# Performance work log

Hardware: AMD Instinct MI355X
Metric: run time of the kernel (lower is better)

Reference implementation:

```python
import jax, jax.numpy as jnp
import numpy as np

N_SITES = 1024
N_SYMM = 1024
ALPHA_SYMM = 16  # alpha * n_sites / n_symm with alpha=16


def logcosh(x):
    # numerically stable log(cosh(x)) = |x| + log1p(exp(-2|x|)) - log(2)
    ax = jnp.abs(x)
    return ax + jnp.log1p(jnp.exp(-2.0 * ax)) - jnp.log(2.0)


def setup_inputs() -> dict:
    key = jax.random.key(0)
    k1, k2, k3, k4 = jax.random.split(key, 4)
    x_in = jax.random.normal(k1, (4096, N_SITES), dtype=jnp.float32)
    Wsymm = jax.random.normal(k2, (N_SITES, ALPHA_SYMM), dtype=jnp.float32) * 0.1
    bsymm = jax.random.normal(k3, (ALPHA_SYMM,), dtype=jnp.float32) * 0.1
    v_bias = jax.random.normal(k4, (1,), dtype=jnp.float32) * 0.1
    # cyclic translation group: perm_i[k] = (k + i) mod n_sites
    perms = (np.arange(N_SITES)[:, None] + np.arange(N_SITES)[None, :]) % N_SITES
    perms = jnp.asarray(perms, dtype=jnp.int32)  # [n_symm, n_sites]
    return {"x_in": x_in, "Wsymm": Wsymm, "bsymm": bsymm, "v_bias": v_bias, "perms": perms}


def reference(x_in, Wsymm, bsymm, v_bias, perms):
    n_symm, n_sites = perms.shape
    # expand_kernel: kernel[i, j*n_sites + k] = Wsymm[perms[i, k], j]
    # Wsymm[perms] -> [n_symm, n_sites, alpha_symm]; transpose and flatten -> [n_symm, alpha_symm*n_sites]
    kernel = jnp.transpose(Wsymm[perms], (0, 2, 1)).reshape(n_symm, -1)
    # expand_bias: repeat each bsymm[j] n_symm times -> [alpha_symm*n_symm]
    bias = jnp.repeat(bsymm, n_symm)
    y = x_in @ kernel + bias  # [batch, n_hidden]
    y = jnp.sum(logcosh(y), axis=-1)  # [batch]
    y = y + v_bias[0] * jnp.sum(x_in, axis=-1)
    return y
```

## Files before the change

kernel.cpp:

```cpp
#include <hip/hip_runtime.h>
#include <hip/hip_bf16.h>
#include <math.h>

#define LN2F 0.6931471805599453f
#define SCL 9.765625e-4f
#define TWO_OVER_LN2 2.885390081777927f

typedef __attribute__((ext_vector_type(2))) float f32x2;


#define LSW(s) ((s) ^ (((s) >> 4) & 15))

__device__ __forceinline__ f32x2 mk2(float x, float y) { f32x2 r; r.x = x; r.y = y; return r; }

__device__ __forceinline__ f32x2 cmul(f32x2 a, f32x2 b) {
  return a.xx * b + mk2(-a.y, a.y) * b.yx;
}

__device__ __forceinline__ f32x2 pk_cmul(f32x2 a, f32x2 b) {
  f32x2 d, t;
  asm("v_pk_mul_f32 %1, %2, %3 op_sel:[0,0] op_sel_hi:[0,1]\n\t"
      "v_pk_fma_f32 %0, %2, %3, %1 op_sel:[1,1,0] op_sel_hi:[1,0,1] neg_lo:[1,0,0]"
      : "=v"(d), "=&v"(t) : "v"(a), "v"(b));
  return d;
}
__device__ __forceinline__ f32x2 pk_cmulj(f32x2 a, f32x2 b) {
  f32x2 d, t;
  asm("v_pk_mul_f32 %1, %2, %3 op_sel:[0,0] op_sel_hi:[0,1] neg_hi:[0,1]\n\t"
      "v_pk_fma_f32 %0, %2, %3, %1 op_sel:[1,1,0] op_sel_hi:[1,0,1]"
      : "=v"(d), "=&v"(t) : "v"(a), "v"(b));
  return d;
}
__device__ __forceinline__ f32x2 pk_add(f32x2 a, f32x2 b) {
  f32x2 o;
  asm("v_pk_add_f32 %0, %1, %2" : "=v"(o) : "v"(a), "v"(b));
  return o;
}
__device__ __forceinline__ f32x2 pk_sub(f32x2 a, f32x2 b) {
  f32x2 o;
  asm("v_pk_add_f32 %0, %1, %2 neg_lo:[0,1] neg_hi:[0,1]" : "=v"(o) : "v"(a), "v"(b));
  return o;
}
__device__ __forceinline__ f32x2 pk_addrot_p(f32x2 a, f32x2 d) {
  f32x2 o;
  asm("v_pk_add_f32 %0, %1, %2 op_sel:[0,1] op_sel_hi:[1,0] neg_lo:[0,1]"
      : "=v"(o) : "v"(a), "v"(d));
  return o;
}
__device__ __forceinline__ f32x2 pk_addrot_m(f32x2 a, f32x2 d) {
  f32x2 o;
  asm("v_pk_add_f32 %0, %1, %2 op_sel:[0,1] op_sel_hi:[1,0] neg_hi:[0,1]"
      : "=v"(o) : "v"(a), "v"(d));
  return o;
}
__device__ __forceinline__ f32x2 pk_nabs(f32x2 a) {
  return mk2(fabsf(a.x), fabsf(a.y));
}

__device__ __forceinline__ float fast_exp2(float x) {
#if __has_builtin(__builtin_amdgcn_exp2f)
  return __builtin_amdgcn_exp2f(x);
#else
  return exp2f(x);
#endif
}
__device__ __forceinline__ float fast_log2(float x) {
#if __has_builtin(__builtin_amdgcn_logf)
  return __builtin_amdgcn_logf(x);
#else
  return __log2f(x);
#endif
}

__device__ __forceinline__ f32x2 Ctw(int m) {
  switch (m) {
    case 0:   return mk2(1.f, 0.f);
    case 1:   return mk2(0.999981175f, -0.006135885f);
    case 2:   return mk2(0.999924702f, -0.012271538f);
    case 3:   return mk2(0.999830582f, -0.018406730f);
    case 64:  return mk2(0.923879533f, -0.382683432f);
    case 128: return mk2(0.707106781f, -0.707106781f);
    case 192: return mk2(0.382683432f, -0.923879533f);
    case 256: return mk2(0.f, -1.f);
    case 384: return mk2(-0.707106781f, -0.707106781f);
    case 576: return mk2(-0.923879533f, 0.382683432f);
  }
  return mk2(1.f, 0.f);
}

#define BFLY_F(x0,x1,x2,x3,W1,W2,W3,y0,y1,y2,y3) do { \
  f32x2 t0 = x0+x2, t1 = x1+x3, t2 = x0-x2, d_ = x1-x3; \
  f32x2 t3 = mk2(d_.y, -d_.x); \
  y0 = t0+t1; y1 = cmul(t2+t3, W1); \
  y2 = cmul(t0-t1, W2); y3 = cmul(t2-t3, W3); } while(0)

#define BFLY_I(x0,x1,x2,x3,W1,W2,W3,y0,y1,y2,y3) do { \
  f32x2 u1 = pk_cmulj(x1,W1), u2 = pk_cmulj(x2,W2), u3 = pk_cmulj(x3,W3); \
  f32x2 t0 = pk_add(x0,u2), t1 = pk_add(u1,u3), t2 = pk_sub(x0,u2), d_ = pk_sub(u1,u3); \
  y0 = pk_add(t0,t1); y1 = pk_addrot_p(t2,d_); \
  y2 = pk_sub(t0,t1); y3 = pk_addrot_m(t2,d_); } while(0)

#define BFLY_I1(x0,x1,x2,x3,y0,y1,y2,y3) do { \
  f32x2 t0 = pk_add(x0,x2), t1 = pk_add(x1,x3), t2 = pk_sub(x0,x2), d_ = pk_sub(x1,x3); \
  y0 = pk_add(t0,t1); y1 = pk_addrot_p(t2,d_); \
  y2 = pk_sub(t0,t1); y3 = pk_addrot_m(t2,d_); } while(0)

__global__ void k_twiddle(f32x2* __restrict__ tw) {
  int m = blockIdx.x * 256 + threadIdx.x;
  float th = (float)(2.0 * M_PI / 1024.0) * (float)m;
  tw[m] = mk2(cosf(th), -sinf(th));
}

__global__ __launch_bounds__(256, 3) void k_fft_fwd(
    const float* __restrict__ src, int estride, int rstride,
    const f32x2* __restrict__ tw, f32x2* __restrict__ dst, float scale,
    const float* __restrict__ vbias, float* __restrict__ out, int dorow) {
  __shared__ __align__(16) f32x2 fft[4][1024];
  int tid = threadIdx.x, wv = tid >> 6, u = tid & 63;
  int row = blockIdx.x * 4 + wv;
  const float* xr = src + (size_t)row * rstride;
  f32x2* L = fft[wv];
  f32x2 twu = tw[u];
  f32x2 tw4u = tw[4 * u];
  int tp = u & 3;
  f32x2 tw16t = tw[16 * tp], tw64t = tw[64 * tp];

  float vr[4][4]; float rs = 0.f;
  #pragma unroll
  for (int a = 0; a < 4; ++a)
    #pragma unroll
    for (int k = 0; k < 4; ++k) {
      float s = xr[(u + 64 * a + 256 * k) * estride];
      vr[a][k] = s; rs += s;
    }
  f32x2 v[4][4];
  #pragma unroll
  for (int a = 0; a < 4; ++a) {
    float x0 = vr[a][0], x1 = vr[a][1], x2 = vr[a][2], x3 = vr[a][3];
    float t0 = x0 + x2, t1 = x1 + x3, t2 = x0 - x2, dm = x1 - x3;
    f32x2 W1 = cmul(twu, Ctw(64 * a));
    f32x2 W2 = cmul(W1, W1), W3 = cmul(W1, W2);
    v[a][0] = mk2(t0 + t1, 0.f);
    v[a][1] = cmul(mk2(t2, -dm), W1);
    v[a][2] = cmul(mk2(t0 - t1, 0.f), W2);
    v[a][3] = cmul(mk2(t2, dm), W3);
  }
  {
    f32x2 W1 = tw4u, W2 = cmul(W1, W1), W3 = cmul(W1, W2);
    #pragma unroll
    for (int k = 0; k < 4; ++k) {
      f32x2 y0,y1,y2,y3;
      BFLY_F(v[0][k], v[1][k], v[2][k], v[3][k], W1, W2, W3, y0,y1,y2,y3);
      v[0][k]=y0; v[1][k]=y1; v[2][k]=y2; v[3][k]=y3;
    }
  }
  #pragma unroll
  for (int a = 0; a < 4; ++a)
    #pragma unroll
    for (int k = 0; k < 4; ++k)
      L[LSW(u + 64 * a + 256 * k)] = v[a][k];

  int D = u >> 2;
  f32x2 w[4][4];
  #pragma unroll
  for (int c = 0; c < 4; ++c)
    #pragma unroll
    for (int ap = 0; ap < 4; ++ap)
      w[c][ap] = L[LSW(64 * D + 16 * c + 4 * ap + tp)];
  #pragma unroll
  for (int ap = 0; ap < 4; ++ap) {
    f32x2 W1 = cmul(Ctw(64 * ap), tw16t);
    f32x2 W2 = cmul(W1, W1), W3 = cmul(W1, W2);
    f32x2 y0,y1,y2,y3;
    BFLY_F(w[0][ap], w[1][ap], w[2][ap], w[3][ap], W1, W2, W3, y0,y1,y2,y3);
    w[0][ap]=y0; w[1][ap]=y1; w[2][ap]=y2; w[3][ap]=y3;
  }
  {
    f32x2 W1 = tw64t, W2 = cmul(W1, W1), W3 = cmul(W1, W2);
    #pragma unroll
    for (int c = 0; c < 4; ++c) {
      f32x2 y0,y1,y2,y3;
      BFLY_F(w[c][0], w[c][1], w[c][2], w[c][3], W1, W2, W3, y0,y1,y2,y3);
      w[c][0]=y0; w[c][1]=y1; w[c][2]=y2; w[c][3]=y3;
    }
  }
  #pragma unroll
  for (int c = 0; c < 4; ++c)
    #pragma unroll
    for (int ap = 0; ap < 4; ++ap)
      L[LSW(64 * D + 16 * c + 4 * ap + tp)] = w[c][ap];

  f32x2* drow = dst + (size_t)row * 1024;
  #pragma unroll
  for (int j = 0; j < 4; ++j) {
    f32x2 z0 = L[LSW(16 * u + 4 * j)];
    f32x2 z1 = L[LSW(16 * u + 4 * j + 1)];
    f32x2 z2 = L[LSW(16 * u + 4 * j + 2)];
    f32x2 z3 = L[LSW(16 * u + 4 * j + 3)];
    f32x2 t0 = z0+z2, t1 = z1+z3, t2 = z0-z2, d = z1-z3;
    f32x2 t3 = mk2(d.y, -d.x);
    f32x2 y0 = (t0+t1)*scale, y1 = (t2+t3)*scale, y2 = (t0-t1)*scale, y3 = (t2-t3)*scale;
    float4* dp = (float4*)(drow + 16 * u + 4 * j);
    dp[0] = make_float4(y0.x, y0.y, y1.x, y1.y);
    dp[1] = make_float4(y2.x, y2.y, y3.x, y3.y);
  }
  if (dorow) {
    #pragma unroll
    for (int m = 32; m; m >>= 1) rs += __shfl_down(rs, m);
    if (u == 0) out[row] = vbias[0] * rs;
  }
}


#define PW(M, XA, XB, ZA, ZB) do { \
  float4 qa = W0p[M], qb = W1p[M]; \
  f32x2 g1 = pk_cmulj(mk2(qa.x,qa.y), XA); \
  f32x2 g2 = pk_cmulj(mk2(qb.x,qb.y), XA); \
  ZA = pk_addrot_p(g1, g2); \
  g1 = pk_cmulj(mk2(qa.z,qa.w), XB); \
  g2 = pk_cmulj(mk2(qb.z,qb.w), XB); \
  ZB = pk_addrot_p(g1, g2); } while(0)

#define QP_A(P, LPA) do { \
  const float4* W0p = (const float4*)(Wfs + (size_t)(2*(P)) * 1024 + s16); \
  const float4* W1p = (const float4*)(Wfs + (size_t)(2*(P) + 1) * 1024 + s16); \
  f32x2 z0,z1,z2,z3,z4,z5,z6,z7,z8,z9,z10,z11,z12,z13,z14,z15; \
  PW(0, xr0, xr1, z0, z1);   PW(1, xr2, xr3, z2, z3); \
  PW(2, xr4, xr5, z4, z5);   PW(3, xr6, xr7, z6, z7); \
  PW(4, xr8, xr9, z8, z9);   PW(5, xr10, xr11, z10, z11); \
  PW(6, xr12, xr13, z12, z13); PW(7, xr14, xr15, z14, z15); \
  BFLY_I1(z0,z1,z2,z3, z0,z1,z2,z3); \
  BFLY_I1(z4,z5,z6,z7, z4,z5,z6,z7); \
  BFLY_I1(z8,z9,z10,z11, z8,z9,z10,z11); \
  BFLY_I1(z12,z13,z14,z15, z12,z13,z14,z15); \
  BFLY_I1(z0,z4,z8,z12, z0,z4,z8,z12); \
  BFLY_I(z1,z5,z9,z13, Ctw(64),Ctw(128),Ctw(192), z1,z5,z9,z13); \
  BFLY_I(z2,z6,z10,z14, Ctw(128),Ctw(256),Ctw(384), z2,z6,z10,z14); \
  BFLY_I(z3,z7,z11,z15, Ctw(192),Ctw(384),Ctw(576), z3,z7,z11,z15); \
  (LPA)[0]=z0;   (LPA)[1]=z1;   (LPA)[2]=z2;   (LPA)[3]=z3; \
  (LPA)[4]=z4;   (LPA)[5]=z5;   (LPA)[6]=z6;   (LPA)[7]=z7; \
  (LPA)[8]=z8;   (LPA)[9]=z9;   (LPA)[10]=z10; (LPA)[11]=z11; \
  (LPA)[12]=z12; (LPA)[13]=z13; (LPA)[14]=z14; (LPA)[15]=z15; \
} while(0)

#define QP_B(LPB) do { \
  f32x2 w00,w01,w02,w03,w10,w11,w12,w13,w20,w21,w22,w23,w30,w31,w32,w33; \
  w00 = (LPB)[0];   w01 = (LPB)[68];  w02 = (LPB)[136]; w03 = (LPB)[204]; \
  w10 = (LPB)[17];  w11 = (LPB)[85];  w12 = (LPB)[153]; w13 = (LPB)[221]; \
  w20 = (LPB)[34];  w21 = (LPB)[102]; w22 = (LPB)[170]; w23 = (LPB)[238]; \
  w30 = (LPB)[51];  w31 = (LPB)[119]; w32 = (LPB)[187]; w33 = (LPB)[255]; \
  BFLY_I(w00,w10,w20,w30, TB1,TB2,TB3, w00,w10,w20,w30); \
  BFLY_I(w01,w11,w21,w31, TB1,TB2,TB3, w01,w11,w21,w31); \
  BFLY_I(w02,w12,w22,w32, TB1,TB2,TB3, w02,w12,w22,w32); \
  BFLY_I(w03,w13,w23,w33, TB1,TB2,TB3, w03,w13,w23,w33); \
  BFLY_I(w00,w01,w02,w03, TC10,TC20,TC30, w00,w01,w02,w03); \
  BFLY_I(w10,w11,w12,w13, TC11,TC21,TC31, w10,w11,w12,w13); \
  BFLY_I(w20,w21,w22,w23, TC12,TC22,TC32, w20,w21,w22,w23); \
  BFLY_I(w30,w31,w32,w33, TC13,TC23,TC33, w30,w31,w32,w33); \
  (LPB)[0]=w00;   (LPB)[68]=w01;  (LPB)[136]=w02; (LPB)[204]=w03; \
  (LPB)[17]=w10;  (LPB)[85]=w11;  (LPB)[153]=w12; (LPB)[221]=w13; \
  (LPB)[34]=w20;  (LPB)[102]=w21; (LPB)[170]=w22; (LPB)[238]=w23; \
  (LPB)[51]=w30;  (LPB)[119]=w31; (LPB)[187]=w32; (LPB)[255]=w33; \
} while(0)

#define LCACC(C) do { \
  f32x2 t2_ = pk_add((C), bias2); \
  f32x2 u2_ = pk_nabs(t2_); \
  accL0 += fast_log2(1.f + fast_exp2(-u2_.x)); \
  accL1 += fast_log2(1.f + fast_exp2(-u2_.y)); \
  accU = pk_add(accU, u2_); } while(0)

#define QPC_PH(LPC, I, T1, T2, T3) do { \
  f32x2 c0 = (LPC)[(I)],     c1 = (LPC)[(I)+272]; \
  f32x2 c2 = (LPC)[(I)+544], c3 = (LPC)[(I)+816]; \
  BFLY_I(c0,c1,c2,c3,T1,T2,T3,c0,c1,c2,c3); \
  LCACC(c0); LCACC(c1); LCACC(c2); LCACC(c3); } while(0)

#define QP_C(LPC) do { \
  QPC_PH(LPC, 0, TD10, TD20, TD30); \
  QPC_PH(LPC, 1, TD11, TD21, TD31); \
  QPC_PH(LPC, 2, TD12, TD22, TD32); \
  QPC_PH(LPC, 3, TD13, TD23, TD33); } while(0)

__global__ __launch_bounds__(512, 4) void k_corr(
    const f32x2* __restrict__ X, const f32x2* __restrict__ Wfs,
    const float* __restrict__ bs, const f32x2* __restrict__ tw,
    float* __restrict__ out) {
  __shared__ __align__(16) f32x2 LBW[8][1088];
  __shared__ float red[8];
  int tid = threadIdx.x, wv = tid >> 6, u = tid & 63;
  int b = blockIdx.x;
  f32x2* L = LBW[wv];
  f32x2* LPA = L + 17 * u;
  f32x2* LPB = L + 272 * (u >> 4) + (u & 15);
  f32x2* LPC = L + 4 * u + (u >> 2);
  f32x2 tw4u = tw[4 * u];
  int t = u & 15;
  f32x2 tw16t = tw[16 * t], tw4t = tw[4 * t];
  int s16 = 16 * u;

  f32x2 xr0,xr1,xr2,xr3,xr4,xr5,xr6,xr7,xr8,xr9,xr10,xr11,xr12,xr13,xr14,xr15;
  {
    const float4* Xp = (const float4*)(X + (size_t)b * 1024 + s16);
    float4 q;
    q = Xp[0]; xr0  = mk2(q.x,q.y); xr1  = mk2(q.z,q.w);
    q = Xp[1]; xr2  = mk2(q.x,q.y); xr3  = mk2(q.z,q.w);
    q = Xp[2]; xr4  = mk2(q.x,q.y); xr5  = mk2(q.z,q.w);
    q = Xp[3]; xr6  = mk2(q.x,q.y); xr7  = mk2(q.z,q.w);
    q = Xp[4]; xr8  = mk2(q.x,q.y); xr9  = mk2(q.z,q.w);
    q = Xp[5]; xr10 = mk2(q.x,q.y); xr11 = mk2(q.z,q.w);
    q = Xp[6]; xr12 = mk2(q.x,q.y); xr13 = mk2(q.z,q.w);
    q = Xp[7]; xr14 = mk2(q.x,q.y); xr15 = mk2(q.z,q.w);
  }
  f32x2 bias2 = mk2(bs[2*wv] * TWO_OVER_LN2, bs[2*wv+1] * TWO_OVER_LN2);

  QP_A(wv, LPA);

  f32x2 TB1 = tw16t, TB2 = pk_cmul(TB1,TB1), TB3 = pk_cmul(TB1,TB2);
  f32x2 TC10 = tw4t,                  TC20 = pk_cmul(TC10,TC10), TC30 = pk_cmul(TC10,TC20);
  f32x2 TC11 = pk_cmul(tw4t,Ctw(64)),  TC21 = pk_cmul(TC11,TC11), TC31 = pk_cmul(TC11,TC21);
  f32x2 TC12 = pk_cmul(tw4t,Ctw(128)), TC22 = pk_cmul(TC12,TC12), TC32 = pk_cmul(TC12,TC22);
  f32x2 TC13 = pk_cmul(tw4t,Ctw(192)), TC23 = pk_cmul(TC13,TC13), TC33 = pk_cmul(TC13,TC23);

  QP_B(LPB);

  f32x2 TD10 = tw4u,                 TD20 = pk_cmul(TD10,TD10), TD30 = pk_cmul(TD10,TD20);
  f32x2 TD11 = pk_cmul(tw4u,Ctw(1)), TD21 = pk_cmul(TD11,TD11), TD31 = pk_cmul(TD11,TD21);
  f32x2 TD12 = pk_cmul(tw4u,Ctw(2)), TD22 = pk_cmul(TD12,TD12), TD32 = pk_cmul(TD12,TD22);
  f32x2 TD13 = pk_cmul(tw4u,Ctw(3)), TD23 = pk_cmul(TD13,TD13), TD33 = pk_cmul(TD13,TD23);

  float accL0 = 0.f, accL1 = 0.f;
  f32x2 accU = mk2(0.f, 0.f);
  QP_C(LPC);

  float acc = (accL0 + accL1) + 0.5f * (accU.x + accU.y);
  #pragma unroll
  for (int m = 32; m; m >>= 1) acc += __shfl_down(acc, m);
  if (u == 0) red[wv] = acc;
  __syncthreads();
  if (tid == 0) {
    float s = ((red[0] + red[1]) + (red[2] + red[3]))
            + ((red[4] + red[5]) + (red[6] + red[7]));
    out[b] += LN2F * (s - 16384.f);
  }
}

__global__ void k_naive(const float* __restrict__ x, const float* __restrict__ W,
                        const float* __restrict__ bs, const float* __restrict__ vb,
                        float* __restrict__ out) {
  int b = blockIdx.x;
  __shared__ float xs[1024];
  __shared__ float red[256];
  int t = threadIdx.x;
  float xsum = 0.f;
  for (int i = t; i < 1024; i += 256) { float v = x[(size_t)b * 1024 + i]; xs[i] = v; xsum += v; }
  __syncthreads();
  float tot = vb[0] * xsum;
  for (int h = t; h < 16384; h += 256) {
    int j = h >> 10, kh = h & 1023;
    float a = bs[j];
    for (int i = 0; i < 1024; ++i) a += xs[i] * W[((i + kh) & 1023) * 16 + j];
    float ax = fabsf(a);
    tot += ax + __logf(1.f + __expf(-2.f * ax)) - LN2F;
  }
  red[t] = tot;
  __syncthreads();
  for (int s2 = 128; s2; s2 >>= 1) { if (t < s2) red[t] += red[t + s2]; __syncthreads(); }
  if (t == 0) out[b] = red[0];
}

extern "C" void kernel_launch(void* const* d_in, const int* in_sizes, int n_in,
                              void* d_out, int out_size, void* d_ws, size_t ws_size,
                              hipStream_t stream) {
  const float* x  = (const float*)d_in[0];
  const float* W  = (const float*)d_in[1];
  const float* bs = (const float*)d_in[2];
  const float* vb = (const float*)d_in[3];
  float* out = (float*)d_out;

  size_t need = 8192 + 131072 + (size_t)4096 * 1024 * 8;
  if (ws_size < need) {
    k_naive<<<4096, 256, 0, stream>>>(x, W, bs, vb, out);
    return;
  }
  f32x2* tw  = (f32x2*)d_ws;
  f32x2* Wfs = (f32x2*)((char*)d_ws + 8192);
  f32x2* X   = (f32x2*)((char*)d_ws + 8192 + 131072);

  k_twiddle<<<4, 256, 0, stream>>>(tw);
  k_fft_fwd<<<4, 256, 0, stream>>>(W, 16, 1, tw, Wfs, SCL * TWO_OVER_LN2, vb, out, 0);
  k_fft_fwd<<<1024, 256, 0, stream>>>(x, 1, 1024, tw, X, 1.0f, vb, out, 1);
  k_corr<<<4096, 512, 0, stream>>>(X, Wfs, bs, tw, out);
}
```

Before: 133.6 us.

## Process two hidden channel pairs per wave and merge log calls via products

k_corr now uses 256 threads per block, and each wave handles two channel pairs (four hidden features) instead of one. The x register data and twiddle setup are reused across both pairs. The log-cosh accumulation multiplies the two (1+exp) factors and takes a single log2, halving the log evaluations. The cost is more per-wave work and register pressure, a lower launch-bounds occupancy target, and a small risk to accuracy from the product.

```diff
diff --git a/kernel.cpp b/kernel.cpp
--- a/kernel.cpp
+++ b/kernel.cpp
@@ -263,37 +263,42 @@
   (LPB)[51]=w30;  (LPB)[119]=w31; (LPB)[187]=w32; (LPB)[255]=w33; \
 } while(0)
 
-#define LCACC(C) do { \
-  f32x2 t2_ = pk_add((C), bias2); \
+#define LCACC(C, B2, ACC) do { \
+  f32x2 t2_ = pk_add((C), (B2)); \
   f32x2 u2_ = pk_nabs(t2_); \
-  accL0 += fast_log2(1.f + fast_exp2(-u2_.x)); \
-  accL1 += fast_log2(1.f + fast_exp2(-u2_.y)); \
+  float p_ = (1.f + fast_exp2(-u2_.x)) * (1.f + fast_exp2(-u2_.y)); \
+  ACC += fast_log2(p_); \
   accU = pk_add(accU, u2_); } while(0)
 
-#define QPC_PH(LPC, I, T1, T2, T3) do { \
+#define QPC_PH(LPC, I, T1, T2, T3, B2) do { \
   f32x2 c0 = (LPC)[(I)],     c1 = (LPC)[(I)+272]; \
   f32x2 c2 = (LPC)[(I)+544], c3 = (LPC)[(I)+816]; \
   BFLY_I(c0,c1,c2,c3,T1,T2,T3,c0,c1,c2,c3); \
-  LCACC(c0); LCACC(c1); LCACC(c2); LCACC(c3); } while(0)
-
-#define QP_C(LPC) do { \
-  QPC_PH(LPC, 0, TD10, TD20, TD30); \
-  QPC_PH(LPC, 1, TD11, TD21, TD31); \
-  QPC_PH(LPC, 2, TD12, TD22, TD32); \
-  QPC_PH(LPC, 3, TD13, TD23, TD33); } while(0)
-
-__global__ __launch_bounds__(512, 4) void k_corr(
+  LCACC(c0, B2, accL0); LCACC(c1, B2, accL1); \
+  LCACC(c2, B2, accL0); LCACC(c3, B2, accL1); } while(0)
+
+#define QP_C(LPC, B2) do { \
+  QPC_PH(LPC, 0, TD10, TD20, TD30, B2); \
+  QPC_PH(LPC, 1, TD11, TD21, TD31, B2); \
+  QPC_PH(LPC, 2, TD12, TD22, TD32, B2); \
+  QPC_PH(LPC, 3, TD13, TD23, TD33, B2); } while(0)
+
+__global__ __launch_bounds__(256, 2) void k_corr(
     const f32x2* __restrict__ X, const f32x2* __restrict__ Wfs,
     const float* __restrict__ bs, const f32x2* __restrict__ tw,
     float* __restrict__ out) {
-  __shared__ __align__(16) f32x2 LBW[8][1088];
-  __shared__ float red[8];
+  __shared__ __align__(16) f32x2 LBW[4][2][1088];
+  __shared__ float red[4];
   int tid = threadIdx.x, wv = tid >> 6, u = tid & 63;
   int b = blockIdx.x;
-  f32x2* L = LBW[wv];
-  f32x2* LPA = L + 17 * u;
-  f32x2* LPB = L + 272 * (u >> 4) + (u & 15);
-  f32x2* LPC = L + 4 * u + (u >> 2);
+  f32x2* L0 = LBW[wv][0];
+  f32x2* L1 = LBW[wv][1];
+  f32x2* LPA0 = L0 + 17 * u;
+  f32x2* LPA1 = L1 + 17 * u;
+  f32x2* LPB0 = L0 + 272 * (u >> 4) + (u & 15);
+  f32x2* LPB1 = L1 + 272 * (u >> 4) + (u & 15);
+  f32x2* LPC0 = L0 + 4 * u + (u >> 2);
+  f32x2* LPC1 = L1 + 4 * u + (u >> 2);
   f32x2 tw4u = tw[4 * u];
   int t = u & 15;
   f32x2 tw16t = tw[16 * t], tw4t = tw[4 * t];
@@ -312,9 +317,11 @@
     q = Xp[6]; xr12 = mk2(q.x,q.y); xr13 = mk2(q.z,q.w);
     q = Xp[7]; xr14 = mk2(q.x,q.y); xr15 = mk2(q.z,q.w);
   }
-  f32x2 bias2 = mk2(bs[2*wv] * TWO_OVER_LN2, bs[2*wv+1] * TWO_OVER_LN2);
-
-  QP_A(wv, LPA);
+  f32x2 bias20 = mk2(bs[4*wv]   * TWO_OVER_LN2, bs[4*wv+1] * TWO_OVER_LN2);
+  f32x2 bias21 = mk2(bs[4*wv+2] * TWO_OVER_LN2, bs[4*wv+3] * TWO_OVER_LN2);
+
+  QP_A(2*wv,     LPA0);
+  QP_A(2*wv + 1, LPA1);
 
   f32x2 TB1 = tw16t, TB2 = pk_cmul(TB1,TB1), TB3 = pk_cmul(TB1,TB2);
   f32x2 TC10 = tw4t,                  TC20 = pk_cmul(TC10,TC10), TC30 = pk_cmul(TC10,TC20);
@@ -322,7 +329,8 @@
   f32x2 TC12 = pk_cmul(tw4t,Ctw(128)), TC22 = pk_cmul(TC12,TC12), TC32 = pk_cmul(TC12,TC22);
   f32x2 TC13 = pk_cmul(tw4t,Ctw(192)), TC23 = pk_cmul(TC13,TC13), TC33 = pk_cmul(TC13,TC23);
 
-  QP_B(LPB);
+  QP_B(LPB0);
+  QP_B(LPB1);
 
   f32x2 TD10 = tw4u,                 TD20 = pk_cmul(TD10,TD10), TD30 = pk_cmul(TD10,TD20);
   f32x2 TD11 = pk_cmul(tw4u,Ctw(1)), TD21 = pk_cmul(TD11,TD11), TD31 = pk_cmul(TD11,TD21);
@@ -331,7 +339,8 @@
 
   float accL0 = 0.f, accL1 = 0.f;
   f32x2 accU = mk2(0.f, 0.f);
-  QP_C(LPC);
+  QP_C(LPC0, bias20);
+  QP_C(LPC1, bias21);
 
   float acc = (accL0 + accL1) + 0.5f * (accU.x + accU.y);
   #pragma unroll
@@ -339,8 +348,7 @@
   if (u == 0) red[wv] = acc;
   __syncthreads();
   if (tid == 0) {
-    float s = ((red[0] + red[1]) + (red[2] + red[3]))
-            + ((red[4] + red[5]) + (red[6] + red[7]));
+    float s = (red[0] + red[1]) + (red[2] + red[3]);
     out[b] += LN2F * (s - 16384.f);
   }
 }
@@ -390,5 +398,5 @@
   k_twiddle<<<4, 256, 0, stream>>>(tw);
   k_fft_fwd<<<4, 256, 0, stream>>>(W, 16, 1, tw, Wfs, SCL * TWO_OVER_LN2, vb, out, 0);
   k_fft_fwd<<<1024, 256, 0, stream>>>(x, 1, 1024, tw, X, 1.0f, vb, out, 1);
-  k_corr<<<4096, 512, 0, stream>>>(X, Wfs, bs, tw, out);
-}
+  k_corr<<<4096, 256, 0, stream>>>(X, Wfs, bs, tw, out);
+}
```

After: 129.1 us, median of 2. -3.3%, faster.
